# Kernel optimization log

Hardware: AMD Instinct MI355X
Metric: run time of the kernel (lower is better)

The kernel has to match this reference:

```python
import jax, jax.numpy as jnp
import numpy as np

K = 3
STRIDE = 1
PAD = 1


def conv2d(x, w, b):
    # standard NCHW conv, stride 1, pad 1
    out = jax.lax.conv_general_dilated(
        x, w, (STRIDE, STRIDE), [(PAD, PAD), (PAD, PAD)],
        dimension_numbers=("NCHW", "OIHW", "NCHW"))
    return out + b[None, :, None, None]


def deform_conv2d(x, offset, mask, weight):
    # torchvision.ops.deform_conv2d semantics (offset_groups=1):
    # offset: [B, 2*K*K, Ho, Wo] laid out as (k, (y, x)) per kernel tap k (row-major)
    # mask:   [B, K*K, Ho, Wo]
    B, C, H, W = x.shape
    KK = K * K
    Ho, Wo = offset.shape[2:]
    off = offset.reshape(B, KK, 2, Ho, Wo)

    # base sampling positions: p = out*stride - pad + kernel_tap + offset
    tap_y = jnp.repeat(jnp.arange(K, dtype=x.dtype), K)  # [KK]
    tap_x = jnp.tile(jnp.arange(K, dtype=x.dtype), K)    # [KK]
    grid_y = jnp.arange(Ho, dtype=x.dtype) * STRIDE - PAD
    grid_x = jnp.arange(Wo, dtype=x.dtype) * STRIDE - PAD
    py = grid_y[None, None, :, None] + tap_y[None, :, None, None] + off[:, :, 0]  # [B,KK,Ho,Wo]
    px = grid_x[None, None, None, :] + tap_x[None, :, None, None] + off[:, :, 1]

    y0 = jnp.floor(py)
    x0 = jnp.floor(px)
    wy1 = py - y0  # fractional parts
    wx1 = px - x0

    xf = x.reshape(B, C, H * W)

    def gather(yi, xi):
        # zero-padding semantics: out-of-bounds corners contribute 0
        valid = (yi >= 0) & (yi <= H - 1) & (xi >= 0) & (xi <= W - 1)
        idx = (jnp.clip(yi, 0, H - 1) * W + jnp.clip(xi, 0, W - 1)).astype(jnp.int32)
        v = jnp.take_along_axis(xf, idx.reshape(B, 1, KK * Ho * Wo), axis=2)
        v = v.reshape(B, C, KK, Ho, Wo)
        return v * valid[:, None].astype(x.dtype)

    e = lambda a: a[:, None]  # [B,KK,Ho,Wo] -> [B,1,KK,Ho,Wo]
    sampled = (gather(y0, x0) * e((1 - wy1) * (1 - wx1))
               + gather(y0, x0 + 1) * e((1 - wy1) * wx1)
               + gather(y0 + 1, x0) * e(wy1 * (1 - wx1))
               + gather(y0 + 1, x0 + 1) * e(wy1 * wx1))
    sampled = sampled * mask[:, None]  # modulated, [B,C,KK,Ho,Wo]

    Cout = weight.shape[0]
    out = jnp.einsum("bckhw,ock->bohw", sampled, weight.reshape(Cout, C, KK))
    return out


def setup_inputs() -> dict:
    key = jax.random.key(0)
    ks = jax.random.split(key, 5)
    B, Cin, Cout, H, W = 4, 128, 256, 64, 64
    x = jax.random.normal(ks[0], (B, Cin, H, W), jnp.float32)
    # offset/modulator convs are zero-init in the module; use small random weights
    # so the deformable sampling path is actually exercised
    offset_w = jax.random.normal(ks[1], (2 * K * K, Cin, K, K), jnp.float32) * 0.02
    offset_b = jax.random.normal(ks[2], (2 * K * K,), jnp.float32) * 0.1
    mod_w = jax.random.normal(ks[3], (K * K, Cin, K, K), jnp.float32) * 0.02
    mod_b = jnp.zeros((K * K,), jnp.float32)
    weight = jax.random.normal(ks[4], (Cout, Cin, K, K), jnp.float32) * (1.0 / np.sqrt(Cin * K * K))
    return {"x": x, "offset_w": offset_w, "offset_b": offset_b,
            "mod_w": mod_w, "mod_b": mod_b, "weight": weight}


def reference(x, offset_w, offset_b, mod_w, mod_b, weight):
    H, W = x.shape[2], x.shape[3]
    max_offset = max(H, W) / 4.0
    offset = jnp.clip(conv2d(x, offset_w, offset_b), -max_offset, max_offset)
    mask = 2.0 * jax.nn.sigmoid(conv2d(x, mod_w, mod_b))
    return deform_conv2d(x, offset, mask, weight)
```

## Files before the change

kernel.cpp:

```cpp
#include <hip/hip_runtime.h>
#include <math.h>

#define CIN   128
#define COUT  256
#define HH    64
#define WW    64
#define BB    4
#define KK    9
#define CK    (CIN*KK)

typedef unsigned short u16;
typedef unsigned int   u32;
using f32x4  = __attribute__((ext_vector_type(4))) float;
using s16x8  = __attribute__((ext_vector_type(8))) short;

__device__ __forceinline__ u16 f2bf(float f) {
    union { float f; u32 u; } v; v.f = f;
    u32 u = v.u;
    u += 0x7FFFu + ((u >> 16) & 1u);
    return (u16)(u >> 16);
}
__device__ __forceinline__ float bfel(s16x8 v, int j) {
    union { u32 u; float f; } c; c.u = ((u32)(u16)v[j]) << 16; return c.f;
}
__device__ __forceinline__ u32 pk2(float a, float b) {
    return (u32)f2bf(a) | ((u32)f2bf(b) << 16);
}

__global__ __launch_bounds__(256)
void prep_all(const float* __restrict__ x, const float* __restrict__ w,
              const float* __restrict__ ow, const float* __restrict__ mw,
              u16* __restrict__ xt, u16* __restrict__ wfrag,
              u16* __restrict__ wofsf) {
    __shared__ u16 T[64][130];
    int blk = blockIdx.x;
    int tid = threadIdx.x;

    if (blk < 256) {
        int b = blk >> 6, y = blk & 63;
        int lane = tid & 63, cw = tid >> 6;
        for (int c = cw; c < 128; c += 4)
            T[lane][c] = f2bf(x[((b * 128 + c) * 64 + y) * 64 + lane]);
        __syncthreads();
        int c = tid & 127;
        for (int p = tid >> 7; p < 64; p += 2)
            xt[((b * 64 + y) * 64 + p) * 128 + c] = T[p][c];
    } else if (blk < 256 + 1152) {
        int i = (blk - 256) * 256 + tid;
        int j     = i & 7;
        int lane  = (i >> 3) & 63;
        int ks    = (i >> 9) & 1;
        int ct    = (i >> 10) & 3;
        int q     = (i >> 12) & 3;
        int chunk = i >> 14;
        int co  = q * 64 + ct * 16 + (lane & 15);
        int k   = chunk * 64 + ks * 32 + (lane >> 4) * 8 + j;
        int tap = k >> 7, c = k & 127;
        wfrag[i] = f2bf(w[co * CK + c * 9 + tap]);
    } else {
        int i = (blk - 1408) * 256 + tid;
        if (i < 32 * CK) {
            int j     = i & 7;
            int lane  = (i >> 3) & 63;
            int ks    = (i >> 9) & 1;
            int t     = (i >> 10) & 1;
            int chunk = i >> 11;
            int co  = t * 16 + (lane & 15);
            int k   = chunk * 64 + ks * 32 + (lane >> 4) * 8 + j;
            int tap = k >> 7, c = k & 127;
            float v = 0.f;
            if (co < 18)      v = ow[co * CK + c * 9 + tap];
            else if (co < 27) v = mw[(co - 18) * CK + c * 9 + tap];
            wofsf[i] = f2bf(v);
        }
    }
}

__global__ __launch_bounds__(512, 4)
void dcn_fused(const u16* __restrict__ xt, const u16* __restrict__ wofsf,
               const float* __restrict__ ob, const float* __restrict__ mb,
               const u16* __restrict__ wfrag, float* __restrict__ out) {
    int blkid = blockIdx.x;
    int xcd = blkid & 7, idx = blkid >> 3;
    int b   = xcd >> 1;
    int ho  = ((xcd & 1) << 5) + (idx >> 1);
    int wo0 = (idx & 1) << 5;
    int tid = threadIdx.x;

    __shared__ __align__(16) u16 Sm[2][32][136];
    __shared__ float s_om[27][32];
    __shared__ int   s_idx[32][KK][4];
    __shared__ float s_wgt[32][KK][4];

    int wv   = tid >> 6, lane = tid & 63;
    int quad = lane >> 4, l16 = lane & 15;
    int gpx  = wv * 4 + (lane >> 4);
    int oct  = lane & 15;

    const u16* xtb = xt + (size_t)b * 4096 * 128;
    const s16x8 vzero = {0,0,0,0,0,0,0,0};

    int pa_ph = wv & 1;
    f32x4 aco[2];
    aco[0] = (f32x4)(0.f); aco[1] = (f32x4)(0.f);

    s16x8 sa;
    auto pa_gather = [&](int tap) {
        int kx = tap % 3;
        int y  = ho - 1 + tap / 3;
        bool yok = (unsigned)y < HH;
        int col = wo0 + gpx + kx - 1;
        bool ok = yok && ((unsigned)col < WW);
        int yc = yok ? y : 0;
        int cc = ((unsigned)col < WW) ? col : 0;
        sa = *(const s16x8*)(xtb + (size_t)(yc * 64 + cc) * 128 + oct * 8);
        if (!ok) sa = vzero;
    };

    pa_gather(0);
    int buf = 0;
    for (int tap = 0; tap < 9; ++tap) {
        *(s16x8*)(&Sm[buf][gpx][oct * 8]) = sa;
        __syncthreads();
        if (tap < 8) pa_gather(tap + 1);

        if (wv < 2) {
            const u16* wc = wofsf + lane * 8;
#pragma unroll
            for (int ks4 = 0; ks4 < 4; ++ks4) {
                int chunkA = tap * 2 + (ks4 >> 1);
                s16x8 bfrag = *(const s16x8*)(&Sm[buf][pa_ph * 16 + l16][ks4 * 32 + quad * 8]);
#pragma unroll
                for (int t = 0; t < 2; ++t) {
                    s16x8 afrag = *(const s16x8*)(wc + ((chunkA * 2 + t) * 2 + (ks4 & 1)) * 512);
                    aco[t] = __builtin_amdgcn_mfma_f32_16x16x32_bf16(afrag, bfrag, aco[t], 0, 0, 0);
                }
            }
        }
        buf ^= 1;
    }
    if (wv < 2) {
#pragma unroll
        for (int t = 0; t < 2; ++t) {
#pragma unroll
            for (int r = 0; r < 4; ++r) {
                int co = t * 16 + quad * 4 + r;
                if (co < 27) {
                    float v = aco[t][r];
                    if (co < 18) {
                        v += ob[co];
                        v = fminf(fmaxf(v, -16.f), 16.f);
                    } else {
                        v += mb[co - 18];
                        v = 2.f / (1.f + expf(-v));
                    }
                    s_om[co][pa_ph * 16 + l16] = v;
                }
            }
        }
    }
    __syncthreads();

    if (tid < 32 * KK) {
        int p = tid / KK, k = tid - (tid / KK) * KK;
        int wo = wo0 + p;
        float offy = s_om[2 * k][p];
        float offx = s_om[2 * k + 1][p];
        float mval = s_om[18 + k][p];

        float py = (float)(ho - 1 + k / 3) + offy;
        float px = (float)(wo - 1 + k % 3) + offx;
        float y0f = floorf(py), x0f = floorf(px);
        float wy1 = py - y0f,  wx1 = px - x0f;
        float wy0 = 1.f - wy1, wx0 = 1.f - wx1;
        int iy0 = (int)y0f, ix0 = (int)x0f;
        int iy1 = iy0 + 1,  ix1 = ix0 + 1;
        bool vy0 = (iy0 >= 0) && (iy0 < HH);
        bool vy1 = (iy1 >= 0) && (iy1 < HH);
        bool vx0 = (ix0 >= 0) && (ix0 < WW);
        bool vx1 = (ix1 >= 0) && (ix1 < WW);
        int cy0 = min(max(iy0, 0), HH - 1), cy1 = min(max(iy1, 0), HH - 1);
        int cx0 = min(max(ix0, 0), WW - 1), cx1 = min(max(ix1, 0), WW - 1);
        s_idx[p][k][0] = (cy0 * WW + cx0) * 128;
        s_idx[p][k][1] = (cy0 * WW + cx1) * 128;
        s_idx[p][k][2] = (cy1 * WW + cx0) * 128;
        s_idx[p][k][3] = (cy1 * WW + cx1) * 128;
        s_wgt[p][k][0] = (vy0 && vx0) ? mval * wy0 * wx0 : 0.f;
        s_wgt[p][k][1] = (vy0 && vx1) ? mval * wy0 * wx1 : 0.f;
        s_wgt[p][k][2] = (vy1 && vx0) ? mval * wy1 * wx0 : 0.f;
        s_wgt[p][k][3] = (vy1 && vx1) ? mval * wy1 * wx1 : 0.f;
    }
    __syncthreads();

    const u16* wq = wfrag + lane * 8;

    f32x4 acc[2][2];
#pragma unroll
    for (int t = 0; t < 2; ++t) { acc[t][0] = (f32x4)(0.f); acc[t][1] = (f32x4)(0.f); }

    s16x8 cr0, cr1, cr2, cr3;
    float gg0, gg1, gg2, gg3;
    auto gatherB = [&](int tap) {
        int i0 = s_idx[gpx][tap][0], i1 = s_idx[gpx][tap][1];
        int i2 = s_idx[gpx][tap][2], i3 = s_idx[gpx][tap][3];
        gg0 = s_wgt[gpx][tap][0]; gg1 = s_wgt[gpx][tap][1];
        gg2 = s_wgt[gpx][tap][2]; gg3 = s_wgt[gpx][tap][3];
        int co8 = oct * 8;
        cr0 = *(const s16x8*)(xtb + i0 + co8);
        cr1 = *(const s16x8*)(xtb + i1 + co8);
        cr2 = *(const s16x8*)(xtb + i2 + co8);
        cr3 = *(const s16x8*)(xtb + i3 + co8);
    };

    gatherB(0);
    buf = 0;
    for (int tap = 0; tap < 9; ++tap) {
        float o[8];
#pragma unroll
        for (int j = 0; j < 8; ++j)
            o[j] = gg0 * bfel(cr0, j) + gg1 * bfel(cr1, j)
                 + gg2 * bfel(cr2, j) + gg3 * bfel(cr3, j);
        uint4 pkv;
        pkv.x = pk2(o[0], o[1]); pkv.y = pk2(o[2], o[3]);
        pkv.z = pk2(o[4], o[5]); pkv.w = pk2(o[6], o[7]);
        *(uint4*)(&Sm[buf][gpx][oct * 8]) = pkv;
        __syncthreads();

        s16x8 af[8];
#pragma unroll
        for (int t = 0; t < 2; ++t)
#pragma unroll
            for (int ks4 = 0; ks4 < 4; ++ks4) {
                int chunkB = tap * 2 + (ks4 >> 1);
                af[t * 4 + ks4] = *(const s16x8*)(
                    wq + ((chunkB * 16 + (wv * 2 + t)) * 2 + (ks4 & 1)) * 512);
            }

        if (tap < 8) gatherB(tap + 1);

#pragma unroll
        for (int ks4 = 0; ks4 < 4; ++ks4) {
            s16x8 bf0 = *(const s16x8*)(&Sm[buf][l16][ks4 * 32 + quad * 8]);
            s16x8 bf1 = *(const s16x8*)(&Sm[buf][16 + l16][ks4 * 32 + quad * 8]);
#pragma unroll
            for (int t = 0; t < 2; ++t) {
                acc[t][0] = __builtin_amdgcn_mfma_f32_16x16x32_bf16(af[t * 4 + ks4], bf0, acc[t][0], 0, 0, 0);
                acc[t][1] = __builtin_amdgcn_mfma_f32_16x16x32_bf16(af[t * 4 + ks4], bf1, acc[t][1], 0, 0, 0);
            }
        }
        buf ^= 1;
    }

#pragma unroll
    for (int t = 0; t < 2; ++t) {
        int cobase = (wv * 2 + t) * 16 + quad * 4;
#pragma unroll
        for (int ph = 0; ph < 2; ++ph) {
#pragma unroll
            for (int r = 0; r < 4; ++r) {
                int co = cobase + r;
                out[((b * COUT + co) * HH + ho) * WW + wo0 + ph * 16 + l16] = acc[t][ph][r];
            }
        }
    }
}

extern "C" void kernel_launch(void* const* d_in, const int* in_sizes, int n_in,
                              void* d_out, int out_size, void* d_ws, size_t ws_size,
                              hipStream_t stream) {
    const float* x  = (const float*)d_in[0];
    const float* ow = (const float*)d_in[1];
    const float* ob = (const float*)d_in[2];
    const float* mw = (const float*)d_in[3];
    const float* mb = (const float*)d_in[4];
    const float* wt = (const float*)d_in[5];

    char* ws = (char*)d_ws;
    u16* wfrag = (u16*)ws;  ws += (size_t)COUT * CK * 2;
    u16* wofsf = (u16*)ws;  ws += (size_t)32 * CK * 2;
    u16* xt    = (u16*)ws;
    float* out = (float*)d_out;

    prep_all<<<1552, 256, 0, stream>>>(x, wt, ow, mw, xt, wfrag, wofsf);

    dcn_fused<<<BB * HH * 2, 512, 0, stream>>>(xt, wofsf, ob, mb, wfrag, out);
}
```

Before: 103.8 us.

## Prefetch gathers two taps ahead and relayout weight fragments per tap and wave

Deepens the software pipeline for both the offset-conv gather and the deformable bilinear gather from one tap ahead to two, using double-buffered register slots and fully unrolled tap loops. The weight fragment layouts are rearranged so each wave's per-tap fragments sit in one contiguous block, which simplifies the addressing. The fp32-to-bf16 packing switches from round-to-nearest-even to plain truncation to save ALU work. In exchange it raises register pressure, which could reduce occupancy, and truncation slightly changes numerical accuracy.

```diff
diff --git a/kernel.cpp b/kernel.cpp
--- a/kernel.cpp
+++ b/kernel.cpp
@@ -23,8 +23,8 @@
 __device__ __forceinline__ float bfel(s16x8 v, int j) {
     union { u32 u; float f; } c; c.u = ((u32)(u16)v[j]) << 16; return c.f;
 }
-__device__ __forceinline__ u32 pk2(float a, float b) {
-    return (u32)f2bf(a) | ((u32)f2bf(b) << 16);
+__device__ __forceinline__ u32 asu(float f) {
+    union { float f; u32 u; } v; v.f = f; return v.u;
 }
 
 __global__ __launch_bounds__(256)
@@ -47,27 +47,27 @@
             xt[((b * 64 + y) * 64 + p) * 128 + c] = T[p][c];
     } else if (blk < 256 + 1152) {
         int i = (blk - 256) * 256 + tid;
-        int j     = i & 7;
-        int lane  = (i >> 3) & 63;
-        int ks    = (i >> 9) & 1;
-        int ct    = (i >> 10) & 3;
-        int q     = (i >> 12) & 3;
-        int chunk = i >> 14;
-        int co  = q * 64 + ct * 16 + (lane & 15);
-        int k   = chunk * 64 + ks * 32 + (lane >> 4) * 8 + j;
-        int tap = k >> 7, c = k & 127;
+        int j    = i & 7;
+        int lane = (i >> 3) & 63;
+        int ks4  = (i >> 9) & 3;
+        int t    = (i >> 11) & 1;
+        int wv   = (i >> 12) & 7;
+        int tap  = i >> 15;
+        int co = (wv * 2 + t) * 16 + (lane & 15);
+        int k  = tap * 128 + ks4 * 32 + (lane >> 4) * 8 + j;
+        int c  = k & 127;
         wfrag[i] = f2bf(w[co * CK + c * 9 + tap]);
     } else {
         int i = (blk - 1408) * 256 + tid;
-        if (i < 32 * CK) {
-            int j     = i & 7;
-            int lane  = (i >> 3) & 63;
-            int ks    = (i >> 9) & 1;
-            int t     = (i >> 10) & 1;
-            int chunk = i >> 11;
-            int co  = t * 16 + (lane & 15);
-            int k   = chunk * 64 + ks * 32 + (lane >> 4) * 8 + j;
-            int tap = k >> 7, c = k & 127;
+        if (i < 9 * 4096) {
+            int j    = i & 7;
+            int lane = (i >> 3) & 63;
+            int ks4  = (i >> 9) & 3;
+            int t    = (i >> 11) & 1;
+            int tap  = i >> 12;
+            int co = t * 16 + (lane & 15);
+            int k  = tap * 128 + ks4 * 32 + (lane >> 4) * 8 + j;
+            int c  = k & 127;
             float v = 0.f;
             if (co < 18)      v = ow[co * CK + c * 9 + tap];
             else if (co < 27) v = mw[(co - 18) * CK + c * 9 + tap];
@@ -104,8 +104,8 @@
     f32x4 aco[2];
     aco[0] = (f32x4)(0.f); aco[1] = (f32x4)(0.f);
 
-    s16x8 sa;
-    auto pa_gather = [&](int tap) {
+    s16x8 sreg[2];
+    auto pa_gather = [&](int tap, int slot) {
         int kx = tap % 3;
         int y  = ho - 1 + tap / 3;
         bool yok = (unsigned)y < HH;
@@ -113,26 +113,28 @@
         bool ok = yok && ((unsigned)col < WW);
         int yc = yok ? y : 0;
         int cc = ((unsigned)col < WW) ? col : 0;
-        sa = *(const s16x8*)(xtb + (size_t)(yc * 64 + cc) * 128 + oct * 8);
-        if (!ok) sa = vzero;
+        s16x8 v = *(const s16x8*)(xtb + (size_t)(yc * 64 + cc) * 128 + oct * 8);
+        sreg[slot] = ok ? v : vzero;
     };
 
-    pa_gather(0);
+    pa_gather(0, 0);
+    pa_gather(1, 1);
     int buf = 0;
+#pragma unroll
     for (int tap = 0; tap < 9; ++tap) {
-        *(s16x8*)(&Sm[buf][gpx][oct * 8]) = sa;
+        int sl = tap & 1;
+        *(s16x8*)(&Sm[buf][gpx][oct * 8]) = sreg[sl];
         __syncthreads();
-        if (tap < 8) pa_gather(tap + 1);
+        if (tap + 2 < 9) pa_gather(tap + 2, sl);
 
         if (wv < 2) {
-            const u16* wc = wofsf + lane * 8;
+            const u16* wc = wofsf + tap * 4096 + lane * 8;
 #pragma unroll
             for (int ks4 = 0; ks4 < 4; ++ks4) {
-                int chunkA = tap * 2 + (ks4 >> 1);
                 s16x8 bfrag = *(const s16x8*)(&Sm[buf][pa_ph * 16 + l16][ks4 * 32 + quad * 8]);
 #pragma unroll
                 for (int t = 0; t < 2; ++t) {
-                    s16x8 afrag = *(const s16x8*)(wc + ((chunkA * 2 + t) * 2 + (ks4 & 1)) * 512);
+                    s16x8 afrag = *(const s16x8*)(wc + (t * 4 + ks4) * 512);
                     aco[t] = __builtin_amdgcn_mfma_f32_16x16x32_bf16(afrag, bfrag, aco[t], 0, 0, 0);
                 }
             }
@@ -192,51 +194,53 @@
     }
     __syncthreads();
 
-    const u16* wq = wfrag + lane * 8;
-
     f32x4 acc[2][2];
 #pragma unroll
     for (int t = 0; t < 2; ++t) { acc[t][0] = (f32x4)(0.f); acc[t][1] = (f32x4)(0.f); }
 
-    s16x8 cr0, cr1, cr2, cr3;
-    float gg0, gg1, gg2, gg3;
-    auto gatherB = [&](int tap) {
+    s16x8 crs[2][4];
+    float gs[2][4];
+    auto gatherB = [&](int tap, int slot) {
         int i0 = s_idx[gpx][tap][0], i1 = s_idx[gpx][tap][1];
         int i2 = s_idx[gpx][tap][2], i3 = s_idx[gpx][tap][3];
-        gg0 = s_wgt[gpx][tap][0]; gg1 = s_wgt[gpx][tap][1];
-        gg2 = s_wgt[gpx][tap][2]; gg3 = s_wgt[gpx][tap][3];
+        gs[slot][0] = s_wgt[gpx][tap][0]; gs[slot][1] = s_wgt[gpx][tap][1];
+        gs[slot][2] = s_wgt[gpx][tap][2]; gs[slot][3] = s_wgt[gpx][tap][3];
         int co8 = oct * 8;
-        cr0 = *(const s16x8*)(xtb + i0 + co8);
-        cr1 = *(const s16x8*)(xtb + i1 + co8);
-        cr2 = *(const s16x8*)(xtb + i2 + co8);
-        cr3 = *(const s16x8*)(xtb + i3 + co8);
+        crs[slot][0] = *(const s16x8*)(xtb + i0 + co8);
+        crs[slot][1] = *(const s16x8*)(xtb + i1 + co8);
+        crs[slot][2] = *(const s16x8*)(xtb + i2 + co8);
+        crs[slot][3] = *(const s16x8*)(xtb + i3 + co8);
     };
 
-    gatherB(0);
+    gatherB(0, 0);
+    gatherB(1, 1);
     buf = 0;
+#pragma unroll
     for (int tap = 0; tap < 9; ++tap) {
+        int sl = tap & 1;
+        float g0 = gs[sl][0], g1 = gs[sl][1], g2 = gs[sl][2], g3 = gs[sl][3];
         float o[8];
 #pragma unroll
         for (int j = 0; j < 8; ++j)
-            o[j] = gg0 * bfel(cr0, j) + gg1 * bfel(cr1, j)
-                 + gg2 * bfel(cr2, j) + gg3 * bfel(cr3, j);
+            o[j] = g0 * bfel(crs[sl][0], j) + g1 * bfel(crs[sl][1], j)
+                 + g2 * bfel(crs[sl][2], j) + g3 * bfel(crs[sl][3], j);
         uint4 pkv;
-        pkv.x = pk2(o[0], o[1]); pkv.y = pk2(o[2], o[3]);
-        pkv.z = pk2(o[4], o[5]); pkv.w = pk2(o[6], o[7]);
+        pkv.x = (asu(o[1]) & 0xFFFF0000u) | (asu(o[0]) >> 16);
+        pkv.y = (asu(o[3]) & 0xFFFF0000u) | (asu(o[2]) >> 16);
+        pkv.z = (asu(o[5]) & 0xFFFF0000u) | (asu(o[4]) >> 16);
+        pkv.w = (asu(o[7]) & 0xFFFF0000u) | (asu(o[6]) >> 16);
         *(uint4*)(&Sm[buf][gpx][oct * 8]) = pkv;
         __syncthreads();
 
+        if (tap + 2 < 9) gatherB(tap + 2, sl);
+
+        const u16* wc = wfrag + (tap * 8 + wv) * 4096 + lane * 8;
         s16x8 af[8];
 #pragma unroll
         for (int t = 0; t < 2; ++t)
 #pragma unroll
-            for (int ks4 = 0; ks4 < 4; ++ks4) {
-                int chunkB = tap * 2 + (ks4 >> 1);
-                af[t * 4 + ks4] = *(const s16x8*)(
-                    wq + ((chunkB * 16 + (wv * 2 + t)) * 2 + (ks4 & 1)) * 512);
-            }
-
-        if (tap < 8) gatherB(tap + 1);
+            for (int ks4 = 0; ks4 < 4; ++ks4)
+                af[t * 4 + ks4] = *(const s16x8*)(wc + (t * 4 + ks4) * 512);
 
 #pragma unroll
         for (int ks4 = 0; ks4 < 4; ++ks4) {
```

Result: no change. 103.6 us (-0.1%).
